# Kernel tuning notes

Hardware: AMD Instinct MI355X
Metric: run time of the kernel (lower is better)

Reference implementation:

```python
import jax, jax.numpy as jnp
import numpy as np

B_, N_, D_ = 2, 2048, 512
E_ = 2 * D_          # d_inner = expand * dim
S_ = 16              # d_state
K_ = 4               # d_conv
R_ = 32              # dt_rank = ceil(dim/16)
C_ = 512             # cond_dim


def setup_inputs() -> dict:
    key = jax.random.key(0)
    ks = jax.random.split(key, 12)
    r = lambda i, sh, s=0.02: jax.random.normal(ks[i], sh, dtype=jnp.float32) * s
    return {
        "x": jax.random.normal(ks[0], (B_, N_, D_), dtype=jnp.float32),
        "cond": jax.random.normal(ks[1], (B_, C_), dtype=jnp.float32),
        "ln_g": jnp.ones((D_,), jnp.float32),
        "ln_b": jnp.zeros((D_,), jnp.float32),
        "W_in": r(2, (D_, 2 * E_)),            # in_proj (no bias)
        "conv_w": r(3, (E_, K_), 0.1),          # depthwise causal conv
        "conv_b": jnp.zeros((E_,), jnp.float32),
        "W_x": r(4, (E_, R_ + 2 * S_)),         # x_proj -> dt,B,C
        "W_dt": r(5, (R_, E_), 0.1),
        "b_dt": jnp.full((E_,), -4.6, jnp.float32),  # softplus(-4.6)~0.01
        "A_log": jnp.log(jnp.broadcast_to(jnp.arange(1, S_ + 1, dtype=jnp.float32), (E_, S_))),
        "D_skip": jnp.ones((E_,), jnp.float32),
        "W_out": r(6, (E_, D_)),                # out_proj (no bias)
        "film_gw": r(7, (C_, D_)),
        "film_gb": jnp.ones((D_,), jnp.float32),
        "film_bw": r(8, (C_, D_)),
        "film_bb": jnp.zeros((D_,), jnp.float32),
    }


def reference(x, cond, ln_g, ln_b, W_in, conv_w, conv_b, W_x, W_dt, b_dt,
              A_log, D_skip, W_out, film_gw, film_gb, film_bw, film_bb):
    # --- LayerNorm ---
    mu = x.mean(-1, keepdims=True)
    var = ((x - mu) ** 2).mean(-1, keepdims=True)
    xn = (x - mu) * jax.lax.rsqrt(var + 1e-5) * ln_g + ln_b

    # --- Mamba ---
    xz = xn @ W_in                                  # [B,N,2E]
    u, z = jnp.split(xz, 2, axis=-1)                # [B,N,E] each
    # causal depthwise conv1d (kernel K_), unrolled over small K
    up = jnp.pad(u, ((0, 0), (K_ - 1, 0), (0, 0)))
    uc = conv_b + sum(up[:, k:k + N_, :] * conv_w[:, k] for k in range(K_))
    uc = jax.nn.silu(uc)                            # [B,N,E]

    x_dbl = uc @ W_x                                # [B,N,R+2S]
    dt, Bm, Cm = jnp.split(x_dbl, [R_, R_ + S_], axis=-1)
    delta = jax.nn.softplus(dt @ W_dt + b_dt)       # [B,N,E]

    A = -jnp.exp(A_log)                             # [E,S]
    dA = jnp.exp(delta[..., None] * A)              # [B,N,E,S]
    dBu = (delta * uc)[..., None] * Bm[:, :, None, :]  # [B,N,E,S]

    def step(h, ins):
        dA_t, dBu_t, C_t = ins                      # [B,E,S],[B,E,S],[B,S]
        h = dA_t * h + dBu_t
        y = jnp.einsum('bes,bs->be', h, C_t)
        return h, y

    h0 = jnp.zeros((x.shape[0], E_, S_), dtype=x.dtype)
    _, ys = jax.lax.scan(step, h0,
                         (dA.swapaxes(0, 1), dBu.swapaxes(0, 1), Cm.swapaxes(0, 1)))
    y = ys.swapaxes(0, 1) + D_skip * uc             # [B,N,E]
    y = y * jax.nn.silu(z)
    out = y @ W_out                                 # [B,N,D]

    # --- FiLM ---
    gamma = cond @ film_gw + film_gb                # [B,D]
    beta = cond @ film_bw + film_bb
    return gamma[:, None, :] * out + beta[:, None, :]
```

## Files before the change

kernel.cpp:

```cpp
#include <hip/hip_runtime.h>
#include <hip/hip_bf16.h>
#include <math.h>

#define B_ 2
#define N_ 2048
#define D_ 512
#define E_ 1024
#define S_ 16
#define R_ 32
#define C_ 512
#define CH_ 32
#define NC_ (N_ / CH_)

using short8 = __attribute__((ext_vector_type(8))) short;
using f32x4  = __attribute__((ext_vector_type(4))) float;
using f32x16 = __attribute__((ext_vector_type(16))) float;

__device__ __forceinline__ short f2bf(float f) {
    union { float f; unsigned u; } x; x.f = f;
    unsigned r = (x.u + 0x7fffu + ((x.u >> 16) & 1u)) >> 16;
    return (short)r;
}
__device__ __forceinline__ float bf2f(short s) {
    union { unsigned u; float f; } x;
    x.u = ((unsigned)(unsigned short)s) << 16;
    return x.f;
}
__device__ __forceinline__ void gl_lds16(const void* g, void* l) {
    __builtin_amdgcn_global_load_lds((const __attribute__((address_space(1))) void*)g,
                                     (__attribute__((address_space(3))) void*)l, 16, 0, 0);
}

__global__ __launch_bounds__(256) void prep_kernel(
    const float* __restrict__ x, float2* __restrict__ stats,
    const float* __restrict__ W_in, short* __restrict__ Wint,
    const float* __restrict__ W_out, short* __restrict__ Woutt,
    const float* __restrict__ W_x, short* __restrict__ Wxt,
    const float* __restrict__ W_dt, short* __restrict__ Wdtt,
    const float* __restrict__ cond,
    const float* __restrict__ gw, const float* __restrict__ gb,
    const float* __restrict__ bw, const float* __restrict__ bb,
    float* __restrict__ gamma, float* __restrict__ beta) {
    __shared__ __align__(16) float smem[2112];
    int bid = blockIdx.x;
    int tid = threadIdx.x;
    if (bid < 8) {
        float* cs = smem;
        float* red = smem + 1024;
        int d0 = bid * 64;
#pragma unroll
        for (int i = tid; i < 2 * C_ / 4; i += 256) {
            int b = i >> 7;
            int c4 = (i & 127) * 4;
            *(float4*)&cs[b * C_ + c4] = *(const float4*)(cond + (size_t)b * C_ + c4);
        }
        __syncthreads();
        int dl = tid & 63, ks = tid >> 6;
        int d = d0 + dl;
        float g0 = 0.f, g1 = 0.f, bt0 = 0.f, bt1 = 0.f;
#pragma unroll 4
        for (int k = ks * 128; k < ks * 128 + 128; k++) {
            float wg = gw[(size_t)k * D_ + d];
            float wb = bw[(size_t)k * D_ + d];
            float c0 = cs[k], c1 = cs[C_ + k];
            g0 = fmaf(c0, wg, g0);
            g1 = fmaf(c1, wg, g1);
            bt0 = fmaf(c0, wb, bt0);
            bt1 = fmaf(c1, wb, bt1);
        }
        red[(ks * 64 + dl) * 4 + 0] = g0; red[(ks * 64 + dl) * 4 + 1] = g1;
        red[(ks * 64 + dl) * 4 + 2] = bt0; red[(ks * 64 + dl) * 4 + 3] = bt1;
        __syncthreads();
        if (ks == 0) {
            float s0 = 0.f, s1 = 0.f, s2 = 0.f, s3 = 0.f;
#pragma unroll
            for (int q = 0; q < 4; q++) {
                s0 += red[(q * 64 + dl) * 4 + 0]; s1 += red[(q * 64 + dl) * 4 + 1];
                s2 += red[(q * 64 + dl) * 4 + 2]; s3 += red[(q * 64 + dl) * 4 + 3];
            }
            float gbv = gb[d], bbv = bb[d];
            gamma[d] = s0 + gbv;
            gamma[D_ + d] = s1 + gbv;
            beta[d] = s2 + bbv;
            beta[D_ + d] = s3 + bbv;
        }
    } else if (bid < 1640) {
        const float* W; short* Wt; int K, N, bx, by;
        int r = bid - 8;
        if (r < 1024)      { W = W_in;  Wt = Wint;  K = 512;  N = 2048; bx = r % 64; by = r / 64; }
        else if (r < 1536) { r -= 1024; W = W_out; Wt = Woutt; K = 1024; N = 512; bx = r % 16; by = r / 16; }
        else if (r < 1600) { r -= 1536; W = W_x;   Wt = Wxt;   K = 1024; N = 64;  bx = r % 2;  by = r / 2; }
        else               { r -= 1600; W = W_dt;  Wt = Wdtt;  K = 32;   N = 1024; bx = r;     by = 0; }
        float (*t)[33] = (float(*)[33])smem;
        int n0 = bx * 32, k0 = by * 32;
        int c = tid & 31, rr0 = tid >> 5;
#pragma unroll
        for (int rr = rr0; rr < 32; rr += 8)
            t[rr][c] = W[(size_t)(k0 + rr) * N + n0 + c];
        __syncthreads();
#pragma unroll
        for (int rr = rr0; rr < 32; rr += 8)
            Wt[(size_t)(n0 + rr) * K + k0 + c] = f2bf(t[c][rr]);
    } else {
        int t = bid - 1640;
        float2 v = *(const float2*)(x + (size_t)t * D_ + tid * 2);
        float s = v.x + v.y;
        float s2 = fmaf(v.x, v.x, v.y * v.y);
#pragma unroll
        for (int o = 32; o >= 1; o >>= 1) {
            s += __shfl_down(s, o);
            s2 += __shfl_down(s2, o);
        }
        int wid = tid >> 6;
        if ((tid & 63) == 0) { smem[wid] = s; smem[4 + wid] = s2; }
        __syncthreads();
        if (tid == 0) {
            float sum = smem[0] + smem[1] + smem[2] + smem[3];
            float sum2 = smem[4] + smem[5] + smem[6] + smem[7];
            float mu = sum * (1.f / (float)D_);
            float var = sum2 * (1.f / (float)D_) - mu * mu;
            stats[t] = make_float2(mu, rsqrtf(var + 1e-5f));
        }
    }
}

template <int BM, int BN, bool FILM, bool LNA, bool OBF>
__global__ __launch_bounds__(256) void gemm_bf16(
    const void* __restrict__ Av, const short* __restrict__ Bt, void* __restrict__ Cv,
    int M, int N, int K,
    const float2* __restrict__ stats, const float* __restrict__ lng, const float* __restrict__ lnb,
    const float* __restrict__ gamma, const float* __restrict__ beta) {
    constexpr int BK = 64;
    constexpr int LDA = LNA ? 72 : 64;
    constexpr int LDB = 64;
    constexpr int WM = BM / 2, WN = BN / 2;
    constexpr int MR = WM / 32, NR = WN / 32;
    __shared__ __align__(16) short As[BM * LDA];
    __shared__ __align__(16) short Bs[BN * LDB];
    int tid = threadIdx.x;
    int lane = tid & 63, w = tid >> 6;
    int wr = w >> 1, wc = w & 1;
    int m0 = blockIdx.y * BM, n0 = blockIdx.x * BN;
    int lr = lane >> 3, lc = lane & 7;

    f32x16 acc[MR][NR];
#pragma unroll
    for (int i = 0; i < MR; i++)
#pragma unroll
        for (int j = 0; j < NR; j++)
#pragma unroll
            for (int r = 0; r < 16; r++) acc[i][j][r] = 0.f;

    int l31 = lane & 31, hk = (lane >> 5) * 8;

    for (int k0 = 0; k0 < K; k0 += BK) {
        __syncthreads();
        if constexpr (LNA) {
            const float* Af = (const float*)Av;
#pragma unroll
            for (int i = tid; i < BM * 8; i += 256) {
                int r = i >> 3, c = (i & 7) * 8;
                float2 st = stats[m0 + r];
                const float* src = Af + (size_t)(m0 + r) * K + k0 + c;
                float4 v0 = *(const float4*)src;
                float4 v1 = *(const float4*)(src + 4);
                float4 g0 = *(const float4*)(lng + k0 + c);
                float4 g1 = *(const float4*)(lng + k0 + c + 4);
                float4 b0 = *(const float4*)(lnb + k0 + c);
                float4 b1 = *(const float4*)(lnb + k0 + c + 4);
                short8 o;
                o[0] = f2bf((v0.x - st.x) * st.y * g0.x + b0.x);
                o[1] = f2bf((v0.y - st.x) * st.y * g0.y + b0.y);
                o[2] = f2bf((v0.z - st.x) * st.y * g0.z + b0.z);
                o[3] = f2bf((v0.w - st.x) * st.y * g0.w + b0.w);
                o[4] = f2bf((v1.x - st.x) * st.y * g1.x + b1.x);
                o[5] = f2bf((v1.y - st.x) * st.y * g1.y + b1.y);
                o[6] = f2bf((v1.z - st.x) * st.y * g1.z + b1.z);
                o[7] = f2bf((v1.w - st.x) * st.y * g1.w + b1.w);
                *(short8*)&As[r * LDA + c] = o;
            }
        } else {
            const short* Ab = (const short*)Av;
#pragma unroll
            for (int ch = w; ch < BM / 8; ch += 4)
                gl_lds16(&Ab[(size_t)(m0 + ch * 8 + lr) * K + k0 + lc * 8], &As[ch * 512]);
        }
#pragma unroll
        for (int ch = w; ch < BN / 8; ch += 4)
            gl_lds16(&Bt[(size_t)(n0 + ch * 8 + lr) * K + k0 + lc * 8], &Bs[ch * 512]);
        __syncthreads();
#pragma unroll
        for (int kk = 0; kk < 4; kk++) {
            short8 a[MR], b[NR];
#pragma unroll
            for (int i = 0; i < MR; i++)
                a[i] = *(const short8*)&As[(wr * WM + i * 32 + l31) * LDA + kk * 16 + hk];
#pragma unroll
            for (int j = 0; j < NR; j++)
                b[j] = *(const short8*)&Bs[(wc * WN + j * 32 + l31) * LDB + kk * 16 + hk];
#pragma unroll
            for (int i = 0; i < MR; i++)
#pragma unroll
                for (int j = 0; j < NR; j++)
                    acc[i][j] = __builtin_amdgcn_mfma_f32_32x32x16_bf16(a[i], b[j], acc[i][j], 0, 0, 0);
        }
    }
    int rbase = 4 * (lane >> 5);
    int bi = m0 >> 11;
#pragma unroll
    for (int i = 0; i < MR; i++)
#pragma unroll
        for (int j = 0; j < NR; j++) {
            int col = n0 + wc * WN + j * 32 + l31;
            float gm = 1.f, bt = 0.f;
            if (FILM) {
                gm = gamma[bi * D_ + col];
                bt = beta[bi * D_ + col];
            }
#pragma unroll
            for (int r = 0; r < 16; r++) {
                int row = m0 + wr * WM + i * 32 + rbase + (r & 3) + 8 * (r >> 2);
                float v = acc[i][j][r];
                if (FILM) v = gm * v + bt;
                if constexpr (OBF)
                    ((short*)Cv)[(size_t)row * N + col] = f2bf(v);
                else
                    ((float*)Cv)[(size_t)row * N + col] = v;
            }
        }
}

__global__ __launch_bounds__(512) void mid_kernel(
    const short* __restrict__ xzb, const float* __restrict__ cw, const float* __restrict__ cb,
    const short* __restrict__ Wxt,
    const short* __restrict__ Wdtt,
    const float* __restrict__ bdt,
    short* __restrict__ ucb, float* __restrict__ xdbl, short* __restrict__ deltab) {
    constexpr int LDU = 1032;
    __shared__ __align__(16) short u[16 * LDU];
    __shared__ __align__(16) float xd2[2][16 * 68];
    int tid = threadIdx.x;
    int t0 = blockIdx.x * 16;
    int n0 = t0 & (N_ - 1);
    {
        int c8 = (tid & 127) * 8;
        int ng = tid >> 7;
        float4 wv[8];
        float cbv[8];
#pragma unroll
        for (int j = 0; j < 8; j++) {
            wv[j] = *(const float4*)(cw + (c8 + j) * 4);
            cbv[j] = cb[c8 + j];
        }
#pragma unroll
        for (int k = 0; k < 4; k++) {
            int n = ng * 4 + k;
            float uf[4][8];
#pragma unroll
            for (int j = 0; j < 4; j++) {
                short8 v = {0, 0, 0, 0, 0, 0, 0, 0};
                if (n0 + n - 3 + j >= 0)
                    v = *(const short8*)&xzb[(size_t)(t0 + n - 3 + j) * (2 * E_) + c8];
#pragma unroll
                for (int q = 0; q < 8; q++) uf[j][q] = bf2f(v[q]);
            }
            short8 o;
#pragma unroll
            for (int q = 0; q < 8; q++) {
                float a = fmaf(wv[q].x, uf[0][q],
                          fmaf(wv[q].y, uf[1][q],
                          fmaf(wv[q].z, uf[2][q],
                          fmaf(wv[q].w, uf[3][q], cbv[q]))));
                float v = a / (1.f + __expf(-a));
                o[q] = f2bf(v);
            }
            *(short8*)&ucb[(size_t)(t0 + n) * E_ + c8] = o;
            *(short8*)&u[n * LDU + c8] = o;
        }
    }
    __syncthreads();
    int lane = tid & 63, w = tid >> 6;
    int cg = w & 3, kh = w >> 2;
    int l15 = lane & 15, kq = (lane >> 4) * 8;
    f32x4 acc4 = {0.f, 0.f, 0.f, 0.f};
#pragma unroll 8
    for (int k0 = 0; k0 < 16; k0++) {
        int kk = kh * 512 + k0 * 32;
        short8 af = *(const short8*)&u[l15 * LDU + kk + kq];
        short8 bfr = *(const short8*)&Wxt[(size_t)(cg * 16 + l15) * E_ + kk + kq];
        acc4 = __builtin_amdgcn_mfma_f32_16x16x32_bf16(af, bfr, acc4, 0, 0, 0);
    }
#pragma unroll
    for (int j = 0; j < 4; j++)
        xd2[kh][((lane >> 4) * 4 + j) * 68 + cg * 16 + l15] = acc4[j];
    __syncthreads();
    if (tid < 256) {
        int r = tid >> 4, c4 = (tid & 15) * 4;
        float4 a = *(const float4*)&xd2[0][r * 68 + c4];
        float4 b = *(const float4*)&xd2[1][r * 68 + c4];
        a.x += b.x; a.y += b.y; a.z += b.z; a.w += b.w;
        *(float4*)&xd2[0][r * 68 + c4] = a;
        *(float4*)&xdbl[(size_t)(t0 + r) * 64 + c4] = a;
    }
    __syncthreads();
    float av[8];
    *(float4*)&av[0] = *(const float4*)&xd2[0][l15 * 68 + kq];
    *(float4*)&av[4] = *(const float4*)&xd2[0][l15 * 68 + kq + 4];
    short8 ab;
#pragma unroll
    for (int j = 0; j < 8; j++) ab[j] = f2bf(av[j]);
    int row4 = (lane >> 4) * 4;
#pragma unroll 4
    for (int t = 0; t < 8; t++) {
        int e = w * 128 + t * 16 + l15;
        short8 bb = *(const short8*)&Wdtt[(size_t)e * 32 + kq];
        f32x4 c4v = {0.f, 0.f, 0.f, 0.f};
        c4v = __builtin_amdgcn_mfma_f32_16x16x32_bf16(ab, bb, c4v, 0, 0, 0);
        float bv = bdt[e];
#pragma unroll
        for (int j = 0; j < 4; j++) {
            float xv = c4v[j] + bv;
            float sp = (xv > 20.f) ? xv : log1pf(__expf(xv));
            deltab[(size_t)(t0 + row4 + j) * E_ + e] = f2bf(sp);
        }
    }
}

__global__ __launch_bounds__(256) void scan_p1(const short* __restrict__ deltab,
                                               const short* __restrict__ ucb,
                                               const float* __restrict__ xdbl,
                                               const float* __restrict__ A_log,
                                               float* __restrict__ hend,
                                               float* __restrict__ cumd) {
    int blk = blockIdx.x;
    int eq = blk & 3;
    int c = (blk >> 2) & (NC_ - 1);
    int b = blk >> 8;
    int tid = threadIdx.x;
    int e = eq * 256 + tid;
    __shared__ float Bsl[CH_][16];
    int base = (b * N_ + c * CH_) * 64;
    for (int i = tid; i < CH_ * 16; i += 256) {
        int n = i >> 4, col = i & 15;
        Bsl[n][col] = xdbl[base + n * 64 + R_ + col];
    }
    float Aes[16];
    const float4* al = (const float4*)(A_log + e * 16);
#pragma unroll
    for (int j = 0; j < 4; j++) {
        float4 a = al[j];
        Aes[j * 4 + 0] = -__expf(a.x);
        Aes[j * 4 + 1] = -__expf(a.y);
        Aes[j * 4 + 2] = -__expf(a.z);
        Aes[j * 4 + 3] = -__expf(a.w);
    }
    __syncthreads();
    float h[16];
#pragma unroll
    for (int s = 0; s < 16; s++) h[s] = 0.f;
    float cum = 0.f;
    const short* dp = deltab + (size_t)(b * N_ + c * CH_) * E_ + e;
    const short* up = ucb + (size_t)(b * N_ + c * CH_) * E_ + e;
#pragma unroll 2
    for (int n = 0; n < CH_; n++) {
        float dv = bf2f(dp[n * E_]);
        float uv = bf2f(up[n * E_]);
        float du = dv * uv;
        cum += dv;
        float Bl[16];
#pragma unroll
        for (int j = 0; j < 4; j++) *(float4*)&Bl[j * 4] = *(const float4*)&Bsl[n][j * 4];
#pragma unroll
        for (int s = 0; s < 16; s++) {
            float dA = __expf(dv * Aes[s]);
            h[s] = fmaf(dA, h[s], du * Bl[s]);
        }
    }
    size_t ob = (size_t)(b * NC_ + c) * 16 * E_ + e;
#pragma unroll
    for (int s = 0; s < 16; s++) hend[ob + (size_t)s * E_] = h[s];
    cumd[(size_t)(b * NC_ + c) * E_ + e] = cum;
}

__global__ __launch_bounds__(256) void scan_comb(float* __restrict__ hend,
                                                 const float* __restrict__ cumd,
                                                 const float* __restrict__ A_log) {
    int idx = blockIdx.x * 256 + threadIdx.x;
    int b = idx >> 14;
    int s = (idx >> 10) & 15;
    int e = idx & 1023;
    float Aes = -__expf(A_log[e * 16 + s]);
    float h = 0.f;
#pragma unroll 4
    for (int c = 0; c < NC_; c++) {
        size_t i = ((size_t)((b * NC_ + c) * 16) + s) * E_ + e;
        float he = hend[i];
        float P = __expf(Aes * cumd[(size_t)(b * NC_ + c) * E_ + e]);
        hend[i] = h;
        h = fmaf(P, h, he);
    }
}

__global__ __launch_bounds__(256) void scan_p3(const short* __restrict__ deltab,
                                               const short* __restrict__ ucb,
                                               const float* __restrict__ xdbl,
                                               const short* __restrict__ xzb,
                                               const float* __restrict__ A_log,
                                               const float* __restrict__ D_skip,
                                               const float* __restrict__ hend,
                                               short* __restrict__ yb) {
    int blk = blockIdx.x;
    int eq = blk & 3;
    int c = (blk >> 2) & (NC_ - 1);
    int b = blk >> 8;
    int tid = threadIdx.x;
    int e = eq * 256 + tid;
    __shared__ float Bsl[CH_][16];
    __shared__ float Csl[CH_][16];
    int base = (b * N_ + c * CH_) * 64;
    for (int i = tid; i < CH_ * 32; i += 256) {
        int n = i >> 5, col = i & 31;
        float v = xdbl[base + n * 64 + R_ + col];
        if (col < 16) Bsl[n][col] = v;
        else Csl[n][col - 16] = v;
    }
    float Aes[16];
    const float4* al = (const float4*)(A_log + e * 16);
#pragma unroll
    for (int j = 0; j < 4; j++) {
        float4 a = al[j];
        Aes[j * 4 + 0] = -__expf(a.x);
        Aes[j * 4 + 1] = -__expf(a.y);
        Aes[j * 4 + 2] = -__expf(a.z);
        Aes[j * 4 + 3] = -__expf(a.w);
    }
    float dsk = D_skip[e];
    float h[16];
    size_t ob = (size_t)(b * NC_ + c) * 16 * E_ + e;
#pragma unroll
    for (int s = 0; s < 16; s++) h[s] = hend[ob + (size_t)s * E_];
    __syncthreads();
    const short* dp = deltab + (size_t)(b * N_ + c * CH_) * E_ + e;
    const short* up = ucb + (size_t)(b * N_ + c * CH_) * E_ + e;
    const short* zp = xzb + (size_t)(b * N_ + c * CH_) * (2 * E_) + E_ + e;
    short* yp = yb + (size_t)(b * N_ + c * CH_) * E_ + e;
#pragma unroll 2
    for (int n = 0; n < CH_; n++) {
        float dv = bf2f(dp[n * E_]);
        float uv = bf2f(up[n * E_]);
        float du = dv * uv;
        float Bl[16], Cl[16];
#pragma unroll
        for (int j = 0; j < 4; j++) {
            *(float4*)&Bl[j * 4] = *(const float4*)&Bsl[n][j * 4];
            *(float4*)&Cl[j * 4] = *(const float4*)&Csl[n][j * 4];
        }
        float y = 0.f;
#pragma unroll
        for (int s = 0; s < 16; s++) {
            float dA = __expf(dv * Aes[s]);
            h[s] = fmaf(dA, h[s], du * Bl[s]);
            y = fmaf(h[s], Cl[s], y);
        }
        float zv = bf2f(zp[n * 2 * E_]);
        float yy = y + dsk * uv;
        yy = yy * (zv / (1.f + __expf(-zv)));
        yp[n * E_] = f2bf(yy);
    }
}

extern "C" void kernel_launch(void* const* d_in, const int* in_sizes, int n_in,
                              void* d_out, int out_size, void* d_ws, size_t ws_size,
                              hipStream_t stream) {
    const float* x       = (const float*)d_in[0];
    const float* cond    = (const float*)d_in[1];
    const float* ln_g    = (const float*)d_in[2];
    const float* ln_b    = (const float*)d_in[3];
    const float* W_in    = (const float*)d_in[4];
    const float* conv_w  = (const float*)d_in[5];
    const float* conv_b  = (const float*)d_in[6];
    const float* W_x     = (const float*)d_in[7];
    const float* W_dt    = (const float*)d_in[8];
    const float* b_dt    = (const float*)d_in[9];
    const float* A_log   = (const float*)d_in[10];
    const float* D_skip  = (const float*)d_in[11];
    const float* W_out   = (const float*)d_in[12];
    const float* film_gw = (const float*)d_in[13];
    const float* film_gb = (const float*)d_in[14];
    const float* film_bw = (const float*)d_in[15];
    const float* film_bb = (const float*)d_in[16];
    float* out = (float*)d_out;

    float* ws = (float*)d_ws;
    float* xdbl  = ws;
    float* gamma = xdbl + 262144;
    float* beta  = gamma + 1024;
    float2* stats = (float2*)(beta + 1024);
    float* hend  = (float*)(stats + 4096);
    float* cumd  = hend + 2097152;
    short* xzb   = (short*)(cumd + 131072);
    short* ucb   = xzb + 8388608;
    short* deltab = ucb + 4194304;
    short* Wint  = deltab + 4194304;
    short* Woutt = Wint + 1048576;
    short* yb    = Woutt + 524288;
    short* Wxt   = yb + 4194304;
    short* Wdtt  = Wxt + 65536;

    prep_kernel<<<5736, 256, 0, stream>>>(
        x, stats, W_in, Wint, W_out, Woutt, W_x, Wxt, W_dt, Wdtt,
        cond, film_gw, film_gb, film_bw, film_bb, gamma, beta);

    gemm_bf16<128, 128, false, true, true>
        <<<dim3(2 * E_ / 128, B_ * N_ / 128), 256, 0, stream>>>(
            x, Wint, xzb, B_ * N_, 2 * E_, D_, stats, ln_g, ln_b, nullptr, nullptr);

    mid_kernel<<<B_ * N_ / 16, 512, 0, stream>>>(
        xzb, conv_w, conv_b, Wxt, Wdtt, b_dt, ucb, xdbl, deltab);

    scan_p1<<<B_ * NC_ * 4, 256, 0, stream>>>(deltab, ucb, xdbl, A_log, hend, cumd);
    scan_comb<<<(B_ * S_ * E_) / 256, 256, 0, stream>>>(hend, cumd, A_log);
    scan_p3<<<B_ * NC_ * 4, 256, 0, stream>>>(deltab, ucb, xdbl, xzb, A_log, D_skip, hend, yb);

    gemm_bf16<128, 64, true, false, false>
        <<<dim3(D_ / 64, B_ * N_ / 128), 256, 0, stream>>>(
            yb, Woutt, out, B_ * N_, D_, E_, nullptr, nullptr, nullptr, gamma, beta);
}
```

Before: 151.3 us.

## Swizzle GEMM tiles across XCDs, reuse conv loads, parallel-scan chunk combine

Three separate changes. The GEMMs move to a 1D grid, with the block index remapped so that consecutive tiles land in contiguous groups for each of the 8 XCDs, which is meant to improve L2 locality. mid_kernel now loads the 7 input rows once per thread group instead of 4 rows per output step, cutting redundant global loads. scan_comb replaces its sequential 64-chunk loop with an LDS-staged, wave-level parallel prefix scan over chunks, which adds shuffles and exps but shortens the dependency chain.

```diff
diff --git a/kernel.cpp b/kernel.cpp
--- a/kernel.cpp
+++ b/kernel.cpp
@@ -140,7 +140,11 @@
     int tid = threadIdx.x;
     int lane = tid & 63, w = tid >> 6;
     int wr = w >> 1, wc = w & 1;
-    int m0 = blockIdx.y * BM, n0 = blockIdx.x * BN;
+    int lid = blockIdx.x;
+    int chunk = gridDim.x >> 3;
+    int swz = (lid & 7) * chunk + (lid >> 3);
+    int ntiles = N / BN;
+    int m0 = (swz / ntiles) * BM, n0 = (swz % ntiles) * BN;
     int lr = lane >> 3, lc = lane & 7;
 
     f32x16 acc[MR][NR];
@@ -244,7 +248,7 @@
     int n0 = t0 & (N_ - 1);
     {
         int c8 = (tid & 127) * 8;
-        int ng = tid >> 7;
+        int base = (tid >> 7) * 4;
         float4 wv[8];
         float cbv[8];
 #pragma unroll
@@ -252,25 +256,25 @@
             wv[j] = *(const float4*)(cw + (c8 + j) * 4);
             cbv[j] = cb[c8 + j];
         }
+        float uf[7][8];
+#pragma unroll
+        for (int j = 0; j < 7; j++) {
+            short8 v = {0, 0, 0, 0, 0, 0, 0, 0};
+            if (n0 + base - 3 + j >= 0)
+                v = *(const short8*)&xzb[(size_t)(t0 + base - 3 + j) * (2 * E_) + c8];
+#pragma unroll
+            for (int q = 0; q < 8; q++) uf[j][q] = bf2f(v[q]);
+        }
 #pragma unroll
         for (int k = 0; k < 4; k++) {
-            int n = ng * 4 + k;
-            float uf[4][8];
-#pragma unroll
-            for (int j = 0; j < 4; j++) {
-                short8 v = {0, 0, 0, 0, 0, 0, 0, 0};
-                if (n0 + n - 3 + j >= 0)
-                    v = *(const short8*)&xzb[(size_t)(t0 + n - 3 + j) * (2 * E_) + c8];
-#pragma unroll
-                for (int q = 0; q < 8; q++) uf[j][q] = bf2f(v[q]);
-            }
+            int n = base + k;
             short8 o;
 #pragma unroll
             for (int q = 0; q < 8; q++) {
-                float a = fmaf(wv[q].x, uf[0][q],
-                          fmaf(wv[q].y, uf[1][q],
-                          fmaf(wv[q].z, uf[2][q],
-                          fmaf(wv[q].w, uf[3][q], cbv[q]))));
+                float a = fmaf(wv[q].x, uf[k][q],
+                          fmaf(wv[q].y, uf[k + 1][q],
+                          fmaf(wv[q].z, uf[k + 2][q],
+                          fmaf(wv[q].w, uf[k + 3][q], cbv[q]))));
                 float v = a / (1.f + __expf(-a));
                 o[q] = f2bf(v);
             }
@@ -385,19 +389,43 @@
 __global__ __launch_bounds__(256) void scan_comb(float* __restrict__ hend,
                                                  const float* __restrict__ cumd,
                                                  const float* __restrict__ A_log) {
-    int idx = blockIdx.x * 256 + threadIdx.x;
-    int b = idx >> 14;
-    int s = (idx >> 10) & 15;
-    int e = idx & 1023;
-    float Aes = -__expf(A_log[e * 16 + s]);
-    float h = 0.f;
+    __shared__ float lh[64][65];
+    __shared__ float lp[64][65];
+    int blk = blockIdx.x;
+    int et = blk & 15;
+    int s = (blk >> 4) & 15;
+    int b = blk >> 8;
+    int e0 = et * 64;
+    int tid = threadIdx.x;
+    int lane = tid & 63, w = tid >> 6;
+    for (int i = tid; i < 64 * 64; i += 256) {
+        int c = i >> 6, e = i & 63;
+        lh[c][e] = hend[((size_t)((b * NC_ + c) * 16) + s) * E_ + e0 + e];
+        lp[c][e] = cumd[(size_t)(b * NC_ + c) * E_ + e0 + e];
+    }
+    __syncthreads();
 #pragma unroll 4
-    for (int c = 0; c < NC_; c++) {
-        size_t i = ((size_t)((b * NC_ + c) * 16) + s) * E_ + e;
-        float he = hend[i];
-        float P = __expf(Aes * cumd[(size_t)(b * NC_ + c) * E_ + e]);
-        hend[i] = h;
-        h = fmaf(P, h, he);
+    for (int q = 0; q < 16; q++) {
+        int e = w * 16 + q;
+        float Aes = -__expf(A_log[(e0 + e) * 16 + s]);
+        float A = __expf(Aes * lp[lane][e]);
+        float Bv = lh[lane][e];
+#pragma unroll
+        for (int off = 1; off < 64; off <<= 1) {
+            float Ap = __shfl_up(A, off);
+            float Bp = __shfl_up(Bv, off);
+            if (lane >= off) {
+                Bv = fmaf(A, Bp, Bv);
+                A *= Ap;
+            }
+        }
+        float hB = __shfl_up(Bv, 1);
+        lh[lane][e] = (lane == 0) ? 0.f : hB;
+    }
+    __syncthreads();
+    for (int i = tid; i < 64 * 64; i += 256) {
+        int c = i >> 6, e = i & 63;
+        hend[((size_t)((b * NC_ + c) * 16) + s) * E_ + e0 + e] = lh[c][e];
     }
 }
 
@@ -512,17 +540,17 @@
         cond, film_gw, film_gb, film_bw, film_bb, gamma, beta);
 
     gemm_bf16<128, 128, false, true, true>
-        <<<dim3(2 * E_ / 128, B_ * N_ / 128), 256, 0, stream>>>(
+        <<<512, 256, 0, stream>>>(
             x, Wint, xzb, B_ * N_, 2 * E_, D_, stats, ln_g, ln_b, nullptr, nullptr);
 
     mid_kernel<<<B_ * N_ / 16, 512, 0, stream>>>(
         xzb, conv_w, conv_b, Wxt, Wdtt, b_dt, ucb, xdbl, deltab);
 
     scan_p1<<<B_ * NC_ * 4, 256, 0, stream>>>(deltab, ucb, xdbl, A_log, hend, cumd);
-    scan_comb<<<(B_ * S_ * E_) / 256, 256, 0, stream>>>(hend, cumd, A_log);
+    scan_comb<<<B_ * S_ * (E_ / 64), 256, 0, stream>>>(hend, cumd, A_log);
     scan_p3<<<B_ * NC_ * 4, 256, 0, stream>>>(deltab, ucb, xdbl, xzb, A_log, D_skip, hend, yb);
 
     gemm_bf16<128, 64, true, false, false>
-        <<<dim3(D_ / 64, B_ * N_ / 128), 256, 0, stream>>>(
+        <<<256, 256, 0, stream>>>(
             yb, Woutt, out, B_ * N_, D_, E_, nullptr, nullptr, nullptr, gamma, beta);
 }
```

After: 144.7 us. 4.3% less time.
